# Optimization experiments

Hardware: AMD Instinct MI355X
Metric: run time of the kernel (lower is better)

## Reference

```python
import jax, jax.numpy as jnp
import numpy as np

B = 2          # number of point clouds (batch vector has B blocks)
N_PER = 16384  # points per cloud
F = 32         # input feature dim
D = 3          # coordinate dim
RATIO = 0.25
R = 0.2        # ball-query radius
K = 64         # max_neighbors
H1 = 64        # MLP hidden
COUT = 128     # MLP output
M = int(N_PER * RATIO)  # centroids per cloud


def setup_inputs() -> dict:
    key = jax.random.key(0)
    k0, k1, k2, k3 = jax.random.split(key, 4)
    x = jax.random.normal(k0, (B * N_PER, F), jnp.float32)
    pos = jax.random.uniform(k1, (B * N_PER, D), jnp.float32)
    batch = jnp.repeat(jnp.arange(B), N_PER)
    W1 = jax.random.normal(k2, (F + D, H1), jnp.float32) / np.sqrt(F + D)
    b1 = jnp.zeros((H1,), jnp.float32)
    W2 = jax.random.normal(k3, (H1, COUT), jnp.float32) / np.sqrt(H1)
    b2 = jnp.zeros((COUT,), jnp.float32)
    return {"x": x, "pos": pos, "batch": batch, "W1": W1, "b1": b1, "W2": W2, "b2": b2}


def _fps(pos_b):
    """Iterative farthest point sampling: (N_PER, D) -> (M,) indices."""
    d0 = jnp.sum((pos_b - pos_b[0]) ** 2, axis=-1)  # start at point 0

    def body(d, _):
        i = jnp.argmax(d)
        d = jnp.minimum(d, jnp.sum((pos_b - pos_b[i]) ** 2, axis=-1))
        return d, i

    _, idxs = jax.lax.scan(body, d0, None, length=M - 1)
    return jnp.concatenate([jnp.zeros((1,), idxs.dtype), idxs])


def _set_abstraction(x_b, pos_b, W1, b1, W2, b2):
    idx = _fps(pos_b)            # (M,)
    pc = pos_b[idx]              # centroid positions (M, D)
    # ball query: squared distances centroids -> all points, capped at K neighbors
    d2 = jnp.sum((pc[:, None, :] - pos_b[None, :, :]) ** 2, axis=-1)  # (M, N_PER)
    neg = jnp.where(d2 <= R * R, -d2, -jnp.inf)
    vals, nbr = jax.lax.top_k(neg, K)        # K nearest within radius
    valid = vals > -jnp.inf                  # (M, K)
    xj = x_b[nbr]                            # (M, K, F)
    pj = pos_b[nbr]                          # (M, K, D)
    # faithful to source: msg = pos_j - pos_i / r  (note: pos_i/r, not (pos_j-pos_i)/r)
    msg = jnp.concatenate([xj, pj - pc[:, None, :] / R], axis=-1)  # (M, K, F+D)
    h = jax.nn.relu(msg @ W1 + b1) @ W2 + b2                       # (M, K, COUT)
    h = jnp.where(valid[:, :, None], h, -jnp.inf)
    out = jnp.max(h, axis=1)                 # max aggregation over neighbors
    out = jnp.where(jnp.isfinite(out), out, 0.0)
    return out, pc


def reference(x, pos, batch, W1, b1, W2, b2):
    xb = x.reshape(B, N_PER, F)
    pb = pos.reshape(B, N_PER, D)
    out, pc = jax.vmap(lambda xx, pp: _set_abstraction(xx, pp, W1, b1, W2, b2))(xb, pb)
    batch_out = jnp.repeat(jnp.arange(B, dtype=batch.dtype), M)
    return out.reshape(B * M, COUT), pc.reshape(B * M, D), batch_out
```

## Files before the change

kernel.cpp:

```cpp
#include <hip/hip_runtime.h>
#include <hip/hip_bf16.h>

#define NPTS 16384
#define MCENT 4096
#define BCLD 2
#define FDIM 32
#define H1DIM 64
#define CODIM 128
#define KNBR 64
#define R2CUT 0.04f

__device__ __forceinline__ float d2e(float ax, float ay, float az,
                                     float bx, float by, float bz) {
  float dx = __fsub_rn(ax, bx);
  float dy = __fsub_rn(ay, by);
  float dz = __fsub_rn(az, bz);
  return __fadd_rn(__fadd_rn(__fmul_rn(dx, dx), __fmul_rn(dy, dy)), __fmul_rn(dz, dz));
}

__device__ __forceinline__ int spread3(int v) {
  return ((v & 4) << 4) | ((v & 2) << 2) | (v & 1);
}
__device__ __forceinline__ int cell_of(float x, float y, float z) {
  int cx = min(7, (int)(x * 8.0f));
  int cy = min(7, (int)(y * 8.0f));
  int cz = min(7, (int)(z * 8.0f));
  return (spread3(cx) << 2) | (spread3(cy) << 1) | spread3(cz);
}

#define DPP_LEXMAX_STEP(bb, nn, ctrl)                                          \
  do {                                                                         \
    unsigned _ob = (unsigned)__builtin_amdgcn_update_dpp(0, (int)(bb), ctrl,   \
                                                         0xf, 0xf, false);     \
    unsigned _on = (unsigned)__builtin_amdgcn_update_dpp(0, (int)(nn), ctrl,   \
                                                         0xf, 0xf, false);     \
    bool _t = (_ob > (bb)) || (_ob == (bb) && _on > (nn));                     \
    (bb) = _t ? _ob : (bb);                                                    \
    (nn) = _t ? _on : (nn);                                                    \
  } while (0)

__device__ __forceinline__ int rdlane(int v, int l) {
  return __builtin_amdgcn_readlane(v, l);
}
__device__ __forceinline__ float rdlanef(float v, int l) {
  return __int_as_float(__builtin_amdgcn_readlane(__float_as_int(v), l));
}

__global__ __launch_bounds__(1024) void fps_kernel(const float* __restrict__ pos,
                                                   int* __restrict__ fps_idx,
                                                   float4* __restrict__ ws_sorted) {
  const int b = blockIdx.x;
  const float* P = pos + (size_t)b * NPTS * 3;
  float4* S = ws_sorted + (size_t)b * NPTS;
  const int tid = threadIdx.x;
  const int lane = tid & 63;
  const int wave = tid >> 6;

  __shared__ int hist[512];
  __shared__ int offs[512];
  __shared__ unsigned long long skey[2][16];
  __shared__ float4 spos[2][16];
  __shared__ int winners[MCENT];

  if (tid < 512) hist[tid] = 0;
  __syncthreads();
#pragma unroll 4
  for (int j = 0; j < 16; ++j) {
    int i = tid + j * 1024;
    float x = P[3 * i + 0], y = P[3 * i + 1], z = P[3 * i + 2];
    atomicAdd(&hist[cell_of(x, y, z)], 1);
  }
  __syncthreads();
  if (tid < 64) {
    int base = tid * 8;
    int loc[8];
    int run = 0;
#pragma unroll
    for (int k = 0; k < 8; ++k) { loc[k] = run; run += hist[base + k]; }
    int inc = run;
#pragma unroll
    for (int off = 1; off < 64; off <<= 1) {
      int o = __shfl_up(inc, off);
      if (tid >= off) inc += o;
    }
    int ex = inc - run;
#pragma unroll
    for (int k = 0; k < 8; ++k) offs[base + k] = ex + loc[k];
  }
  __syncthreads();
#pragma unroll 4
  for (int j = 0; j < 16; ++j) {
    int i = tid + j * 1024;
    float x = P[3 * i + 0], y = P[3 * i + 1], z = P[3 * i + 2];
    int p = atomicAdd(&offs[cell_of(x, y, z)], 1);
    S[p] = make_float4(x, y, z, __int_as_float(i));
  }
  __syncthreads();

  float px[16], py[16], pz[16], d[16];
  unsigned nidx[16];
  const float x0 = P[0], y0 = P[1], z0 = P[2];
  float bxm, bxM, bym, byM, bzm, bzM;
  unsigned tb = 0u, tn = 0u;
  float tx = 0.f, ty = 0.f, tz = 0.f;
#pragma unroll
  for (int j = 0; j < 16; ++j) {
    float4 v = S[tid * 16 + j];
    px[j] = v.x; py[j] = v.y; pz[j] = v.z;
    nidx[j] = ~(unsigned)__float_as_int(v.w);
    float dj = d2e(v.x, v.y, v.z, x0, y0, z0);
    d[j] = dj;
    if (j == 0) {
      bxm = v.x; bxM = v.x; bym = v.y; byM = v.y; bzm = v.z; bzM = v.z;
    } else {
      bxm = fminf(bxm, v.x); bxM = fmaxf(bxM, v.x);
      bym = fminf(bym, v.y); byM = fmaxf(byM, v.y);
      bzm = fminf(bzm, v.z); bzM = fmaxf(bzM, v.z);
    }
    unsigned db = __float_as_uint(dj);
    unsigned nj = nidx[j];
    bool t = (db > tb) || (db == tb && nj > tn);
    tb = t ? db : tb; tn = t ? nj : tn;
    tx = t ? v.x : tx; ty = t ? v.y : ty; tz = t ? v.z : tz;
  }

  if (tid == 0) winners[0] = 0;

  bool wavedirty = true;
  unsigned cwb = 0u, cwn = 0u;
  float cwx = 0.f, cwy = 0.f, cwz = 0.f;

  for (int m = 1; m < MCENT; ++m) {
    const int par = m & 1;

    if (wavedirty) {
      unsigned bb = tb, nn = tn;
      DPP_LEXMAX_STEP(bb, nn, 0x111);
      DPP_LEXMAX_STEP(bb, nn, 0x112);
      DPP_LEXMAX_STEP(bb, nn, 0x114);
      DPP_LEXMAX_STEP(bb, nn, 0x118);
      DPP_LEXMAX_STEP(bb, nn, 0x142);
      DPP_LEXMAX_STEP(bb, nn, 0x143);
      cwb = (unsigned)rdlane((int)bb, 63);
      cwn = (unsigned)rdlane((int)nn, 63);
      unsigned long long own = __ballot(tb == cwb && tn == cwn);
      int ol = (int)__ffsll(own) - 1;
      cwx = rdlanef(tx, ol);
      cwy = rdlanef(ty, ol);
      cwz = rdlanef(tz, ol);
    }
    if (lane == 0) {
      skey[par][wave] = ((unsigned long long)cwb << 32) | (unsigned long long)cwn;
      spos[par][wave] = make_float4(cwx, cwy, cwz, 0.0f);
    }
    __syncthreads();

    unsigned rb, rn;
    unsigned sb0 = 0u, sn0 = 0u;
    {
      unsigned bb = 0u, nn = 0u;
      if (lane < 16) {
        unsigned long long kk = skey[par][lane];
        bb = (unsigned)(kk >> 32);
        nn = (unsigned)kk;
        sb0 = bb; sn0 = nn;
        DPP_LEXMAX_STEP(bb, nn, 0x111);
        DPP_LEXMAX_STEP(bb, nn, 0x112);
        DPP_LEXMAX_STEP(bb, nn, 0x114);
        DPP_LEXMAX_STEP(bb, nn, 0x118);
      }
      rb = (unsigned)rdlane((int)bb, 15);
      rn = (unsigned)rdlane((int)nn, 15);
    }
    unsigned long long wm = __ballot(lane < 16 && sb0 == rb && sn0 == rn);
    int ws = (int)__ffsll(wm) - 1;
    float4 wp = spos[par][ws];
    if (tid == 0) winners[m] = (int)(~rn);

    float ex = fmaxf(fmaxf(bxm - wp.x, wp.x - bxM), 0.0f);
    float ey = fmaxf(fmaxf(bym - wp.y, wp.y - byM), 0.0f);
    float ez = fmaxf(fmaxf(bzm - wp.z, wp.z - bzM), 0.0f);
    float lb = (ex * ex + ey * ey + ez * ez) * 0.999f;
    bool mydirty = lb < __uint_as_float(tb);
    if (mydirty) {
      unsigned nb = 0u, nn2 = 0u;
      float nx = 0.f, ny = 0.f, nz = 0.f;
#pragma unroll
      for (int j = 0; j < 16; ++j) {
        float dj = fminf(d[j], d2e(px[j], py[j], pz[j], wp.x, wp.y, wp.z));
        d[j] = dj;
        unsigned db = __float_as_uint(dj);
        unsigned nj = nidx[j];
        bool t = (db > nb) || (db == nb && nj > nn2);
        nb = t ? db : nb; nn2 = t ? nj : nn2;
        nx = t ? px[j] : nx; ny = t ? py[j] : ny; nz = t ? pz[j] : nz;
      }
      tb = nb; tn = nn2; tx = nx; ty = ny; tz = nz;
    }
    wavedirty = (__ballot(mydirty) != 0ULL);
  }

  __syncthreads();
  for (int i = tid; i < MCENT; i += 1024) fps_idx[b * MCENT + i] = winners[i];
}

__global__ __launch_bounds__(256) void ballq_kernel(const float* __restrict__ pos,
                                                    const int* __restrict__ fps_idx,
                                                    int* __restrict__ nbr,
                                                    float* __restrict__ out_pc,
                                                    float* __restrict__ out_batch) {
  const int wave = threadIdx.x >> 6;
  const int lane = threadIdx.x & 63;
  const int c = blockIdx.x * 4 + wave;
  const int b = c >> 12;
  const float* P = pos + (size_t)b * NPTS * 3;

  const int ci = fps_idx[c];
  const float cx = P[3 * ci + 0];
  const float cy = P[3 * ci + 1];
  const float cz = P[3 * ci + 2];
  if (lane == 0) {
    out_pc[3 * c + 0] = cx;
    out_pc[3 * c + 1] = cy;
    out_pc[3 * c + 2] = cz;
    out_batch[c] = (float)b;
  }

  __shared__ unsigned long long list[4][1024];
  __shared__ int cnt[4];
  if (lane == 0) cnt[wave] = 0;

  for (int i = lane; i < NPTS; i += 64) {
    const float qx = P[3 * i + 0];
    const float qy = P[3 * i + 1];
    const float qz = P[3 * i + 2];
    const float dd = d2e(cx, cy, cz, qx, qy, qz);
    if (dd <= R2CUT) {
      int p = atomicAdd(&cnt[wave], 1);
      if (p < 1024)
        list[wave][p] = ((unsigned long long)__float_as_uint(dd) << 32)
                      | (unsigned long long)(unsigned)i;
    }
  }
  __syncthreads();

  int n = cnt[wave];
  if (n > 1024) n = 1024;

  unsigned long long loc[16];
#pragma unroll
  for (int k = 0; k < 16; ++k) {
    int i = lane + k * 64;
    loc[k] = (i < n) ? list[wave][i] : ~0ULL;
  }
  unsigned long long mv = loc[0];
#pragma unroll
  for (int k = 1; k < 16; ++k)
    if (loc[k] < mv) mv = loc[k];

  int myout = -1;
  for (int s = 0; s < 64; ++s) {
    unsigned long long wmin = mv;
#pragma unroll
    for (int off = 32; off >= 1; off >>= 1) {
      unsigned long long o = __shfl_xor(wmin, off);
      if (o < wmin) wmin = o;
    }
    if (lane == s) myout = (wmin == ~0ULL) ? -1 : (int)(unsigned)wmin;
    if (mv == wmin && wmin != ~0ULL) {
#pragma unroll
      for (int k = 0; k < 16; ++k)
        if (loc[k] == wmin) loc[k] = ~0ULL;
      mv = loc[0];
#pragma unroll
      for (int k = 1; k < 16; ++k)
        if (loc[k] < mv) mv = loc[k];
    }
  }
  nbr[c * KNBR + lane] = myout;
}

__global__ __launch_bounds__(256) void mlp_kernel(const float* __restrict__ pos,
                                                  const float* __restrict__ x,
                                                  const int* __restrict__ fps_idx,
                                                  const int* __restrict__ nbr,
                                                  const float* __restrict__ W1,
                                                  const float* __restrict__ b1,
                                                  const float* __restrict__ W2,
                                                  const float* __restrict__ b2,
                                                  float* __restrict__ out) {
  const int c = blockIdx.x;
  const int b = c >> 12;
  const float* P = pos + (size_t)b * NPTS * 3;
  const float* X = x + (size_t)b * NPTS * FDIM;

  __shared__ float W1s[35 * 64];
  __shared__ float W2s[64 * 128];
  __shared__ float b1s[64];
  __shared__ float b2s[128];
  __shared__ float h1s[64][64];
  __shared__ float pmax[2][128];
  __shared__ int validk[64];

  const int tid = threadIdx.x;
  for (int i = tid; i < 35 * 64; i += 256) W1s[i] = W1[i];
  for (int i = tid; i < 64 * 128; i += 256) W2s[i] = W2[i];
  if (tid < 64) b1s[tid] = b1[tid];
  else if (tid < 192) b2s[tid - 64] = b2[tid - 64];

  const int ci = fps_idx[c];
  const float c5x = P[3 * ci + 0] / 0.2f;
  const float c5y = P[3 * ci + 1] / 0.2f;
  const float c5z = P[3 * ci + 2] / 0.2f;

  const int k = tid >> 2, q = tid & 3;
  const int nk = nbr[c * KNBR + k];
  if (q == 0) validk[k] = (nk >= 0) ? 1 : 0;
  const int nkc = (nk < 0) ? 0 : nk;

  float msg[35];
  const float4* Xr = (const float4*)(X + (size_t)nkc * FDIM);
#pragma unroll
  for (int i4 = 0; i4 < 8; ++i4) {
    float4 v = Xr[i4];
    msg[i4 * 4 + 0] = v.x; msg[i4 * 4 + 1] = v.y;
    msg[i4 * 4 + 2] = v.z; msg[i4 * 4 + 3] = v.w;
  }
  msg[32] = P[3 * nkc + 0] - c5x;
  msg[33] = P[3 * nkc + 1] - c5y;
  msg[34] = P[3 * nkc + 2] - c5z;

  __syncthreads();

  float acc[16];
#pragma unroll
  for (int h = 0; h < 16; ++h) acc[h] = b1s[q * 16 + h];
#pragma unroll
  for (int i = 0; i < 35; ++i) {
    const float m = msg[i];
    const float4* wrow = (const float4*)&W1s[i * 64 + q * 16];
#pragma unroll
    for (int j4 = 0; j4 < 4; ++j4) {
      float4 w = wrow[j4];
      acc[j4 * 4 + 0] += m * w.x;
      acc[j4 * 4 + 1] += m * w.y;
      acc[j4 * 4 + 2] += m * w.z;
      acc[j4 * 4 + 3] += m * w.w;
    }
  }
#pragma unroll
  for (int h = 0; h < 16; ++h) h1s[k][q * 16 + h] = fmaxf(acc[h], 0.0f);
  __syncthreads();

  const int ch = tid & 127, half = tid >> 7;
  float w2r[64];
#pragma unroll
  for (int i = 0; i < 64; ++i) w2r[i] = W2s[i * 128 + ch];

  float mx = -INFINITY;
  for (int k2 = half * 32; k2 < half * 32 + 32; ++k2) {
    if (!validk[k2]) continue;
    float s = b2s[ch];
    const float4* hr = (const float4*)h1s[k2];
#pragma unroll
    for (int i4 = 0; i4 < 16; ++i4) {
      float4 h4 = hr[i4];
      s += h4.x * w2r[i4 * 4 + 0] + h4.y * w2r[i4 * 4 + 1]
         + h4.z * w2r[i4 * 4 + 2] + h4.w * w2r[i4 * 4 + 3];
    }
    mx = fmaxf(mx, s);
  }
  pmax[half][ch] = mx;
  __syncthreads();

  if (tid < 128) {
    float m2 = fmaxf(pmax[0][tid], pmax[1][tid]);
    out[(size_t)c * CODIM + tid] = (m2 > -INFINITY) ? m2 : 0.0f;
  }
}

extern "C" void kernel_launch(void* const* d_in, const int* in_sizes, int n_in,
                              void* d_out, int out_size, void* d_ws, size_t ws_size,
                              hipStream_t stream) {
  const float* x   = (const float*)d_in[0];
  const float* pos = (const float*)d_in[1];
  const float* W1  = (const float*)d_in[3];
  const float* b1  = (const float*)d_in[4];
  const float* W2  = (const float*)d_in[5];
  const float* b2  = (const float*)d_in[6];
  float* out = (float*)d_out;

  int* fps_idx = (int*)d_ws;
  int* nbr     = (int*)d_ws + BCLD * MCENT;
  float4* ws_sorted = (float4*)nbr;

  float* out_pc    = out + (size_t)BCLD * MCENT * CODIM;
  float* out_batch = out_pc + (size_t)BCLD * MCENT * 3;

  hipLaunchKernelGGL(fps_kernel, dim3(BCLD), dim3(1024), 0, stream, pos, fps_idx, ws_sorted);
  hipLaunchKernelGGL(ballq_kernel, dim3(BCLD * MCENT / 4), dim3(256), 0, stream,
                     pos, fps_idx, nbr, out_pc, out_batch);
  hipLaunchKernelGGL(mlp_kernel, dim3(BCLD * MCENT), dim3(256), 0, stream,
                     pos, x, fps_idx, nbr, W1, b1, W2, b2, out);
}
```

Baseline: 7.661 ms.

## Shrink FPS block to 256 threads with 64 points per thread in sub-boxes

The farthest-point-sampling kernel now runs 256 threads (4 waves) per cloud instead of 1024, each thread holding 64 sorted points split into four 16-point sub-blocks, each with its own bounding box and cached max. The cross-wave reduction per iteration shrinks from 16 to 4 entries, aiming to cut barrier and LDS reduction cost on the serial 4095-step loop, and per-sub-block bounding-box pruning skips distance updates for distant sub-blocks. Point indices are packed as 16-bit values to save registers. In exchange each thread does more sequential work when its sub-blocks are dirty, and register pressure is much higher (64-element arrays), which risks spills.

```diff
diff --git a/kernel.cpp b/kernel.cpp
--- a/kernel.cpp
+++ b/kernel.cpp
@@ -46,9 +46,9 @@
   return __int_as_float(__builtin_amdgcn_readlane(__float_as_int(v), l));
 }
 
-__global__ __launch_bounds__(1024) void fps_kernel(const float* __restrict__ pos,
-                                                   int* __restrict__ fps_idx,
-                                                   float4* __restrict__ ws_sorted) {
+__global__ __launch_bounds__(256, 1) void fps_kernel(const float* __restrict__ pos,
+                                                     int* __restrict__ fps_idx,
+                                                     float4* __restrict__ ws_sorted) {
   const int b = blockIdx.x;
   const float* P = pos + (size_t)b * NPTS * 3;
   float4* S = ws_sorted + (size_t)b * NPTS;
@@ -58,15 +58,16 @@
 
   __shared__ int hist[512];
   __shared__ int offs[512];
-  __shared__ unsigned long long skey[2][16];
-  __shared__ float4 spos[2][16];
+  __shared__ unsigned long long skey[2][4];
+  __shared__ float4 spos[2][4];
   __shared__ int winners[MCENT];
 
-  if (tid < 512) hist[tid] = 0;
+  hist[tid] = 0;
+  hist[tid + 256] = 0;
   __syncthreads();
 #pragma unroll 4
-  for (int j = 0; j < 16; ++j) {
-    int i = tid + j * 1024;
+  for (int j = 0; j < 64; ++j) {
+    int i = tid + j * 256;
     float x = P[3 * i + 0], y = P[3 * i + 1], z = P[3 * i + 2];
     atomicAdd(&hist[cell_of(x, y, z)], 1);
   }
@@ -89,39 +90,61 @@
   }
   __syncthreads();
 #pragma unroll 4
-  for (int j = 0; j < 16; ++j) {
-    int i = tid + j * 1024;
+  for (int j = 0; j < 64; ++j) {
+    int i = tid + j * 256;
     float x = P[3 * i + 0], y = P[3 * i + 1], z = P[3 * i + 2];
     int p = atomicAdd(&offs[cell_of(x, y, z)], 1);
     S[p] = make_float4(x, y, z, __int_as_float(i));
   }
   __syncthreads();
 
-  float px[16], py[16], pz[16], d[16];
-  unsigned nidx[16];
+  float px[64], py[64], pz[64], d[64];
+  unsigned npk[32];
+  unsigned long long skmax[4];
+  float sbxm[4], sbxM[4], sbym[4], sbyM[4], sbzm[4], sbzM[4];
+  float spxr[4], spyr[4], spzr[4];
   const float x0 = P[0], y0 = P[1], z0 = P[2];
-  float bxm, bxM, bym, byM, bzm, bzM;
-  unsigned tb = 0u, tn = 0u;
-  float tx = 0.f, ty = 0.f, tz = 0.f;
-#pragma unroll
-  for (int j = 0; j < 16; ++j) {
-    float4 v = S[tid * 16 + j];
-    px[j] = v.x; py[j] = v.y; pz[j] = v.z;
-    nidx[j] = ~(unsigned)__float_as_int(v.w);
-    float dj = d2e(v.x, v.y, v.z, x0, y0, z0);
-    d[j] = dj;
-    if (j == 0) {
-      bxm = v.x; bxM = v.x; bym = v.y; byM = v.y; bzm = v.z; bzM = v.z;
-    } else {
-      bxm = fminf(bxm, v.x); bxM = fmaxf(bxM, v.x);
-      bym = fminf(bym, v.y); byM = fmaxf(byM, v.y);
-      bzm = fminf(bzm, v.z); bzM = fmaxf(bzM, v.z);
-    }
-    unsigned db = __float_as_uint(dj);
-    unsigned nj = nidx[j];
-    bool t = (db > tb) || (db == tb && nj > tn);
-    tb = t ? db : tb; tn = t ? nj : tn;
-    tx = t ? v.x : tx; ty = t ? v.y : ty; tz = t ? v.z : tz;
+
+#pragma unroll
+  for (int s = 0; s < 4; ++s) {
+    unsigned sb = 0u, sn = 0u;
+    float sx = 0.f, sy = 0.f, sz = 0.f;
+    float xm = 1e30f, xM = -1e30f, ym = 1e30f, yM = -1e30f, zm = 1e30f, zM = -1e30f;
+#pragma unroll
+    for (int t = 0; t < 16; ++t) {
+      const int j = s * 16 + t;
+      float4 v = S[tid * 64 + j];
+      px[j] = v.x; py[j] = v.y; pz[j] = v.z;
+      unsigned nj = ~(unsigned)__float_as_int(v.w);
+      if ((j & 1) == 0) npk[j >> 1] = nj & 0xFFFFu;
+      else npk[j >> 1] |= (nj & 0xFFFFu) << 16;
+      float dj = d2e(v.x, v.y, v.z, x0, y0, z0);
+      d[j] = dj;
+      xm = fminf(xm, v.x); xM = fmaxf(xM, v.x);
+      ym = fminf(ym, v.y); yM = fmaxf(yM, v.y);
+      zm = fminf(zm, v.z); zM = fmaxf(zM, v.z);
+      unsigned db = __float_as_uint(dj);
+      bool g = (db > sb) || (db == sb && nj > sn);
+      sb = g ? db : sb; sn = g ? nj : sn;
+      sx = g ? v.x : sx; sy = g ? v.y : sy; sz = g ? v.z : sz;
+    }
+    skmax[s] = ((unsigned long long)sb << 32) | sn;
+    sbxm[s] = xm; sbxM[s] = xM; sbym[s] = ym; sbyM[s] = yM; sbzm[s] = zm; sbzM[s] = zM;
+    spxr[s] = sx; spyr[s] = sy; spzr[s] = sz;
+  }
+
+  unsigned tkb, tkn;
+  float tx, ty, tz;
+  {
+    unsigned long long k = skmax[0];
+    float ax = spxr[0], ay = spyr[0], az = spzr[0];
+#pragma unroll
+    for (int s = 1; s < 4; ++s) {
+      bool g = skmax[s] > k;
+      k = g ? skmax[s] : k;
+      ax = g ? spxr[s] : ax; ay = g ? spyr[s] : ay; az = g ? spzr[s] : az;
+    }
+    tkb = (unsigned)(k >> 32); tkn = (unsigned)k; tx = ax; ty = ay; tz = az;
   }
 
   if (tid == 0) winners[0] = 0;
@@ -134,7 +157,7 @@
     const int par = m & 1;
 
     if (wavedirty) {
-      unsigned bb = tb, nn = tn;
+      unsigned bb = tkb, nn = tkn;
       DPP_LEXMAX_STEP(bb, nn, 0x111);
       DPP_LEXMAX_STEP(bb, nn, 0x112);
       DPP_LEXMAX_STEP(bb, nn, 0x114);
@@ -143,7 +166,7 @@
       DPP_LEXMAX_STEP(bb, nn, 0x143);
       cwb = (unsigned)rdlane((int)bb, 63);
       cwn = (unsigned)rdlane((int)nn, 63);
-      unsigned long long own = __ballot(tb == cwb && tn == cwn);
+      unsigned long long own = __ballot(tkb == cwb && tkn == cwn);
       int ol = (int)__ffsll(own) - 1;
       cwx = rdlanef(tx, ol);
       cwy = rdlanef(ty, ol);
@@ -159,49 +182,64 @@
     unsigned sb0 = 0u, sn0 = 0u;
     {
       unsigned bb = 0u, nn = 0u;
-      if (lane < 16) {
+      if (lane < 4) {
         unsigned long long kk = skey[par][lane];
         bb = (unsigned)(kk >> 32);
         nn = (unsigned)kk;
         sb0 = bb; sn0 = nn;
         DPP_LEXMAX_STEP(bb, nn, 0x111);
         DPP_LEXMAX_STEP(bb, nn, 0x112);
-        DPP_LEXMAX_STEP(bb, nn, 0x114);
-        DPP_LEXMAX_STEP(bb, nn, 0x118);
       }
-      rb = (unsigned)rdlane((int)bb, 15);
-      rn = (unsigned)rdlane((int)nn, 15);
-    }
-    unsigned long long wm = __ballot(lane < 16 && sb0 == rb && sn0 == rn);
+      rb = (unsigned)rdlane((int)bb, 3);
+      rn = (unsigned)rdlane((int)nn, 3);
+    }
+    unsigned long long wm = __ballot(lane < 4 && sb0 == rb && sn0 == rn);
     int ws = (int)__ffsll(wm) - 1;
     float4 wp = spos[par][ws];
     if (tid == 0) winners[m] = (int)(~rn);
 
-    float ex = fmaxf(fmaxf(bxm - wp.x, wp.x - bxM), 0.0f);
-    float ey = fmaxf(fmaxf(bym - wp.y, wp.y - byM), 0.0f);
-    float ez = fmaxf(fmaxf(bzm - wp.z, wp.z - bzM), 0.0f);
-    float lb = (ex * ex + ey * ey + ez * ez) * 0.999f;
-    bool mydirty = lb < __uint_as_float(tb);
+    bool mydirty = false;
+#pragma unroll
+    for (int s = 0; s < 4; ++s) {
+      float ex = fmaxf(fmaxf(sbxm[s] - wp.x, wp.x - sbxM[s]), 0.0f);
+      float ey = fmaxf(fmaxf(sbym[s] - wp.y, wp.y - sbyM[s]), 0.0f);
+      float ez = fmaxf(fmaxf(sbzm[s] - wp.z, wp.z - sbzM[s]), 0.0f);
+      float lb = (ex * ex + ey * ey + ez * ez) * 0.999f;
+      if (lb < __uint_as_float((unsigned)(skmax[s] >> 32))) {
+        mydirty = true;
+        unsigned nb = 0u, nn2 = 0u;
+        float nx = 0.f, ny = 0.f, nz = 0.f;
+#pragma unroll
+        for (int t = 0; t < 16; ++t) {
+          const int j = s * 16 + t;
+          float dj = fminf(d[j], d2e(px[j], py[j], pz[j], wp.x, wp.y, wp.z));
+          d[j] = dj;
+          unsigned db = __float_as_uint(dj);
+          unsigned nj = 0xFFFF0000u | ((npk[j >> 1] >> ((j & 1) * 16)) & 0xFFFFu);
+          bool g = (db > nb) || (db == nb && nj > nn2);
+          nb = g ? db : nb; nn2 = g ? nj : nn2;
+          nx = g ? px[j] : nx; ny = g ? py[j] : ny; nz = g ? pz[j] : nz;
+        }
+        skmax[s] = ((unsigned long long)nb << 32) | nn2;
+        spxr[s] = nx; spyr[s] = ny; spzr[s] = nz;
+      }
+    }
     if (mydirty) {
-      unsigned nb = 0u, nn2 = 0u;
-      float nx = 0.f, ny = 0.f, nz = 0.f;
-#pragma unroll
-      for (int j = 0; j < 16; ++j) {
-        float dj = fminf(d[j], d2e(px[j], py[j], pz[j], wp.x, wp.y, wp.z));
-        d[j] = dj;
-        unsigned db = __float_as_uint(dj);
-        unsigned nj = nidx[j];
-        bool t = (db > nb) || (db == nb && nj > nn2);
-        nb = t ? db : nb; nn2 = t ? nj : nn2;
-        nx = t ? px[j] : nx; ny = t ? py[j] : ny; nz = t ? pz[j] : nz;
+      unsigned long long k = skmax[0];
+      float ax = spxr[0], ay = spyr[0], az = spzr[0];
+#pragma unroll
+      for (int s = 1; s < 4; ++s) {
+        bool g = skmax[s] > k;
+        k = g ? skmax[s] : k;
+        ax = g ? spxr[s] : ax; ay = g ? spyr[s] : ay; az = g ? spzr[s] : az;
       }
-      tb = nb; tn = nn2; tx = nx; ty = ny; tz = nz;
+      tkb = (unsigned)(k >> 32); tkn = (unsigned)k; tx = ax; ty = ay; tz = az;
     }
     wavedirty = (__ballot(mydirty) != 0ULL);
   }
 
   __syncthreads();
-  for (int i = tid; i < MCENT; i += 1024) fps_idx[b * MCENT + i] = winners[i];
+  for (int i = tid; i < MCENT; i += 256) fps_idx[b * MCENT + i] = winners[i];
 }
 
 __global__ __launch_bounds__(256) void ballq_kernel(const float* __restrict__ pos,
@@ -397,7 +435,7 @@
   float* out_pc    = out + (size_t)BCLD * MCENT * CODIM;
   float* out_batch = out_pc + (size_t)BCLD * MCENT * 3;
 
-  hipLaunchKernelGGL(fps_kernel, dim3(BCLD), dim3(1024), 0, stream, pos, fps_idx, ws_sorted);
+  hipLaunchKernelGGL(fps_kernel, dim3(BCLD), dim3(256), 0, stream, pos, fps_idx, ws_sorted);
   hipLaunchKernelGGL(ballq_kernel, dim3(BCLD * MCENT / 4), dim3(256), 0, stream,
                      pos, fps_idx, nbr, out_pc, out_batch);
   hipLaunchKernelGGL(mlp_kernel, dim3(BCLD * MCENT), dim3(256), 0, stream,
```

Result: slower. 29.81 ms (+289.1%).

## Split FPS into sort kernel and single-wave FPS with lazy subset updates

Applied to the files above, without the earlier changes.

Farthest point sampling moves from a 1024-thread block that needs a __syncthreads per iteration to a single 64-lane wave per cloud. Distances live in LDS, and each lane tracks two 128-point spatially sorted subsets with bounding boxes. Each iteration recomputes only the subsets whose box lower bound says the new centroid can shrink their maximum, so block-wide barriers and most distance updates are skipped. The trade-off is that one wave per cloud leaves almost the whole GPU idle, and dirty subsets are processed one at a time in a serial loop. That could be slower if many subsets need updating per iteration.

```diff
diff --git a/kernel.cpp b/kernel.cpp
--- a/kernel.cpp
+++ b/kernel.cpp
@@ -39,6 +39,16 @@
     (nn) = _t ? _on : (nn);                                                    \
   } while (0)
 
+#define DPP_LEXMAX_FULL(bb, nn)                                                \
+  do {                                                                         \
+    DPP_LEXMAX_STEP(bb, nn, 0x111);                            \
+    DPP_LEXMAX_STEP(bb, nn, 0x112);                            \
+    DPP_LEXMAX_STEP(bb, nn, 0x114);                            \
+    DPP_LEXMAX_STEP(bb, nn, 0x118);                            \
+    DPP_LEXMAX_STEP(bb, nn, 0x142);                          \
+    DPP_LEXMAX_STEP(bb, nn, 0x143);   \
+  } while (0)
+
 __device__ __forceinline__ int rdlane(int v, int l) {
   return __builtin_amdgcn_readlane(v, l);
 }
@@ -46,21 +56,17 @@
   return __int_as_float(__builtin_amdgcn_readlane(__float_as_int(v), l));
 }
 
-__global__ __launch_bounds__(1024) void fps_kernel(const float* __restrict__ pos,
-                                                   int* __restrict__ fps_idx,
-                                                   float4* __restrict__ ws_sorted) {
+__global__ __launch_bounds__(1024) void sort_kernel(const float* __restrict__ pos,
+                                                    float4* __restrict__ Sall,
+                                                    unsigned* __restrict__ umeta,
+                                                    float* __restrict__ fmeta) {
   const int b = blockIdx.x;
   const float* P = pos + (size_t)b * NPTS * 3;
-  float4* S = ws_sorted + (size_t)b * NPTS;
+  float4* S = Sall + (size_t)b * NPTS;
   const int tid = threadIdx.x;
-  const int lane = tid & 63;
-  const int wave = tid >> 6;
 
   __shared__ int hist[512];
   __shared__ int offs[512];
-  __shared__ unsigned long long skey[2][16];
-  __shared__ float4 spos[2][16];
-  __shared__ int winners[MCENT];
 
   if (tid < 512) hist[tid] = 0;
   __syncthreads();
@@ -97,111 +103,147 @@
   }
   __syncthreads();
 
-  float px[16], py[16], pz[16], d[16];
-  unsigned nidx[16];
+  if (tid < 128) {
+    const float x0 = P[0], y0 = P[1], z0 = P[2];
+    unsigned kb = 0u, kn = 0u;
+    float bpx = 0.f, bpy = 0.f, bpz = 0.f;
+    float xm = 1e30f, xM = -1e30f, ym = 1e30f, yM = -1e30f, zm = 1e30f, zM = -1e30f;
+    const float4* Ss = S + tid * 128;
+    for (int t = 0; t < 128; ++t) {
+      float4 v = Ss[t];
+      float dj = d2e(v.x, v.y, v.z, x0, y0, z0);
+      xm = fminf(xm, v.x); xM = fmaxf(xM, v.x);
+      ym = fminf(ym, v.y); yM = fmaxf(yM, v.y);
+      zm = fminf(zm, v.z); zM = fmaxf(zM, v.z);
+      unsigned db = __float_as_uint(dj);
+      unsigned nj = ~(unsigned)__float_as_int(v.w);
+      bool g = (db > kb) || (db == kb && nj > kn);
+      kb = g ? db : kb; kn = g ? nj : kn;
+      bpx = g ? v.x : bpx; bpy = g ? v.y : bpy; bpz = g ? v.z : bpz;
+    }
+    const int gi = b * 128 + tid;
+    umeta[0 * 256 + gi] = kb;
+    umeta[1 * 256 + gi] = kn;
+    fmeta[0 * 256 + gi] = bpx;
+    fmeta[1 * 256 + gi] = bpy;
+    fmeta[2 * 256 + gi] = bpz;
+    fmeta[3 * 256 + gi] = xm;
+    fmeta[4 * 256 + gi] = xM;
+    fmeta[5 * 256 + gi] = ym;
+    fmeta[6 * 256 + gi] = yM;
+    fmeta[7 * 256 + gi] = zm;
+    fmeta[8 * 256 + gi] = zM;
+  }
+}
+
+__global__ __launch_bounds__(64) void fps_wave(const float* __restrict__ pos,
+                                               int* __restrict__ fps_idx,
+                                               const float4* __restrict__ Sall,
+                                               const unsigned* __restrict__ umeta,
+                                               const float* __restrict__ fmeta) {
+  const int b = blockIdx.x;
+  const int lane = threadIdx.x;
+  const float* P = pos + (size_t)b * NPTS * 3;
+  const float4* Sb = Sall + (size_t)b * NPTS;
+
+  __shared__ float dL[NPTS];
+
   const float x0 = P[0], y0 = P[1], z0 = P[2];
-  float bxm, bxM, bym, byM, bzm, bzM;
-  unsigned tb = 0u, tn = 0u;
-  float tx = 0.f, ty = 0.f, tz = 0.f;
-#pragma unroll
-  for (int j = 0; j < 16; ++j) {
-    float4 v = S[tid * 16 + j];
-    px[j] = v.x; py[j] = v.y; pz[j] = v.z;
-    nidx[j] = ~(unsigned)__float_as_int(v.w);
-    float dj = d2e(v.x, v.y, v.z, x0, y0, z0);
-    d[j] = dj;
-    if (j == 0) {
-      bxm = v.x; bxM = v.x; bym = v.y; byM = v.y; bzm = v.z; bzM = v.z;
-    } else {
-      bxm = fminf(bxm, v.x); bxM = fmaxf(bxM, v.x);
-      bym = fminf(bym, v.y); byM = fmaxf(byM, v.y);
-      bzm = fminf(bzm, v.z); bzM = fmaxf(bzM, v.z);
-    }
-    unsigned db = __float_as_uint(dj);
-    unsigned nj = nidx[j];
-    bool t = (db > tb) || (db == tb && nj > tn);
-    tb = t ? db : tb; tn = t ? nj : tn;
-    tx = t ? v.x : tx; ty = t ? v.y : ty; tz = t ? v.z : tz;
-  }
-
-  if (tid == 0) winners[0] = 0;
-
-  bool wavedirty = true;
-  unsigned cwb = 0u, cwn = 0u;
-  float cwx = 0.f, cwy = 0.f, cwz = 0.f;
+#pragma unroll 4
+  for (int it = 0; it < 256; ++it) {
+    int i = it * 64 + lane;
+    float4 v = Sb[i];
+    dL[i] = d2e(v.x, v.y, v.z, x0, y0, z0);
+  }
+
+  unsigned skb[2], skn[2];
+  float spx[2], spy[2], spz[2];
+  float bxm[2], bxM[2], bym[2], byM[2], bzm[2], bzM[2];
+#pragma unroll
+  for (int s2 = 0; s2 < 2; ++s2) {
+    const int gi = b * 128 + lane * 2 + s2;
+    skb[s2] = umeta[0 * 256 + gi];
+    skn[s2] = umeta[1 * 256 + gi];
+    spx[s2] = fmeta[0 * 256 + gi];
+    spy[s2] = fmeta[1 * 256 + gi];
+    spz[s2] = fmeta[2 * 256 + gi];
+    bxm[s2] = fmeta[3 * 256 + gi];
+    bxM[s2] = fmeta[4 * 256 + gi];
+    bym[s2] = fmeta[5 * 256 + gi];
+    byM[s2] = fmeta[6 * 256 + gi];
+    bzm[s2] = fmeta[7 * 256 + gi];
+    bzM[s2] = fmeta[8 * 256 + gi];
+  }
+
+  if (lane == 0) fps_idx[b * MCENT] = 0;
 
   for (int m = 1; m < MCENT; ++m) {
-    const int par = m & 1;
-
-    if (wavedirty) {
-      unsigned bb = tb, nn = tn;
-      DPP_LEXMAX_STEP(bb, nn, 0x111);
-      DPP_LEXMAX_STEP(bb, nn, 0x112);
-      DPP_LEXMAX_STEP(bb, nn, 0x114);
-      DPP_LEXMAX_STEP(bb, nn, 0x118);
-      DPP_LEXMAX_STEP(bb, nn, 0x142);
-      DPP_LEXMAX_STEP(bb, nn, 0x143);
-      cwb = (unsigned)rdlane((int)bb, 63);
-      cwn = (unsigned)rdlane((int)nn, 63);
-      unsigned long long own = __ballot(tb == cwb && tn == cwn);
-      int ol = (int)__ffsll(own) - 1;
-      cwx = rdlanef(tx, ol);
-      cwy = rdlanef(ty, ol);
-      cwz = rdlanef(tz, ol);
-    }
-    if (lane == 0) {
-      skey[par][wave] = ((unsigned long long)cwb << 32) | (unsigned long long)cwn;
-      spos[par][wave] = make_float4(cwx, cwy, cwz, 0.0f);
-    }
-    __syncthreads();
-
-    unsigned rb, rn;
-    unsigned sb0 = 0u, sn0 = 0u;
-    {
-      unsigned bb = 0u, nn = 0u;
-      if (lane < 16) {
-        unsigned long long kk = skey[par][lane];
-        bb = (unsigned)(kk >> 32);
-        nn = (unsigned)kk;
-        sb0 = bb; sn0 = nn;
-        DPP_LEXMAX_STEP(bb, nn, 0x111);
-        DPP_LEXMAX_STEP(bb, nn, 0x112);
-        DPP_LEXMAX_STEP(bb, nn, 0x114);
-        DPP_LEXMAX_STEP(bb, nn, 0x118);
+    bool g2 = (skb[1] > skb[0]) || (skb[1] == skb[0] && skn[1] > skn[0]);
+    unsigned lkb = g2 ? skb[1] : skb[0];
+    unsigned lkn = g2 ? skn[1] : skn[0];
+    float lpx = g2 ? spx[1] : spx[0];
+    float lpy = g2 ? spy[1] : spy[0];
+    float lpz = g2 ? spz[1] : spz[0];
+
+    unsigned bb = lkb, nn = lkn;
+    DPP_LEXMAX_FULL(bb, nn);
+    const unsigned Whi = (unsigned)rdlane((int)bb, 63);
+    const unsigned Wlo = (unsigned)rdlane((int)nn, 63);
+    if (lane == 0) fps_idx[b * MCENT + m] = (int)(~Wlo);
+
+    unsigned long long own = __ballot(lkb == Whi && lkn == Wlo);
+    const int ol = (int)__ffsll(own) - 1;
+    const float wx = rdlanef(lpx, ol);
+    const float wy = rdlanef(lpy, ol);
+    const float wz = rdlanef(lpz, ol);
+
+    unsigned dm = 0u;
+#pragma unroll
+    for (int s2 = 0; s2 < 2; ++s2) {
+      float ex = fmaxf(fmaxf(bxm[s2] - wx, wx - bxM[s2]), 0.0f);
+      float ey = fmaxf(fmaxf(bym[s2] - wy, wy - byM[s2]), 0.0f);
+      float ez = fmaxf(fmaxf(bzm[s2] - wz, wz - bzM[s2]), 0.0f);
+      float lb = (ex * ex + ey * ey + ez * ez) * 0.999f;
+      if (lb < __uint_as_float(skb[s2])) dm |= (1u << s2);
+    }
+
+    unsigned long long anyb = __ballot(dm != 0u);
+    while (anyb) {
+      const int L = (int)__ffsll(anyb) - 1;
+      const unsigned f = (unsigned)rdlane((int)dm, L);
+      const int sl = (f & 1u) ? 0 : 1;
+      const int Ssub = L * 2 + sl;
+      const int pt = Ssub * 128 + lane;
+      float4 v0 = Sb[pt];
+      float4 v1 = Sb[pt + 64];
+      float n0 = fminf(dL[pt],      d2e(v0.x, v0.y, v0.z, wx, wy, wz));
+      float n1 = fminf(dL[pt + 64], d2e(v1.x, v1.y, v1.z, wx, wy, wz));
+      dL[pt] = n0;
+      dL[pt + 64] = n1;
+      unsigned c0b = __float_as_uint(n0), c0n = ~(unsigned)__float_as_int(v0.w);
+      unsigned c1b = __float_as_uint(n1), c1n = ~(unsigned)__float_as_int(v1.w);
+      bool gg = (c1b > c0b) || (c1b == c0b && c1n > c0n);
+      unsigned cb = gg ? c1b : c0b, cn = gg ? c1n : c0n;
+      float cx = gg ? v1.x : v0.x;
+      float cy = gg ? v1.y : v0.y;
+      float cz = gg ? v1.z : v0.z;
+      unsigned b2 = cb, n2 = cn;
+      DPP_LEXMAX_FULL(b2, n2);
+      const unsigned nhi = (unsigned)rdlane((int)b2, 63);
+      const unsigned nlo = (unsigned)rdlane((int)n2, 63);
+      unsigned long long mmk = __ballot(cb == nhi && cn == nlo);
+      const int fl = (int)__ffsll(mmk) - 1;
+      const float nx = rdlanef(cx, fl);
+      const float ny = rdlanef(cy, fl);
+      const float nz = rdlanef(cz, fl);
+      if (lane == L) {
+        skb[sl] = nhi; skn[sl] = nlo;
+        spx[sl] = nx; spy[sl] = ny; spz[sl] = nz;
+        dm &= ~(1u << sl);
       }
-      rb = (unsigned)rdlane((int)bb, 15);
-      rn = (unsigned)rdlane((int)nn, 15);
-    }
-    unsigned long long wm = __ballot(lane < 16 && sb0 == rb && sn0 == rn);
-    int ws = (int)__ffsll(wm) - 1;
-    float4 wp = spos[par][ws];
-    if (tid == 0) winners[m] = (int)(~rn);
-
-    float ex = fmaxf(fmaxf(bxm - wp.x, wp.x - bxM), 0.0f);
-    float ey = fmaxf(fmaxf(bym - wp.y, wp.y - byM), 0.0f);
-    float ez = fmaxf(fmaxf(bzm - wp.z, wp.z - bzM), 0.0f);
-    float lb = (ex * ex + ey * ey + ez * ez) * 0.999f;
-    bool mydirty = lb < __uint_as_float(tb);
-    if (mydirty) {
-      unsigned nb = 0u, nn2 = 0u;
-      float nx = 0.f, ny = 0.f, nz = 0.f;
-#pragma unroll
-      for (int j = 0; j < 16; ++j) {
-        float dj = fminf(d[j], d2e(px[j], py[j], pz[j], wp.x, wp.y, wp.z));
-        d[j] = dj;
-        unsigned db = __float_as_uint(dj);
-        unsigned nj = nidx[j];
-        bool t = (db > nb) || (db == nb && nj > nn2);
-        nb = t ? db : nb; nn2 = t ? nj : nn2;
-        nx = t ? px[j] : nx; ny = t ? py[j] : ny; nz = t ? pz[j] : nz;
-      }
-      tb = nb; tn = nn2; tx = nx; ty = ny; tz = nz;
-    }
-    wavedirty = (__ballot(mydirty) != 0ULL);
-  }
-
-  __syncthreads();
-  for (int i = tid; i < MCENT; i += 1024) fps_idx[b * MCENT + i] = winners[i];
+      anyb = __ballot(dm != 0u);
+    }
+  }
 }
 
 __global__ __launch_bounds__(256) void ballq_kernel(const float* __restrict__ pos,
@@ -391,13 +433,19 @@
   float* out = (float*)d_out;
 
   int* fps_idx = (int*)d_ws;
-  int* nbr     = (int*)d_ws + BCLD * MCENT;
-  float4* ws_sorted = (float4*)nbr;
+  char* region = (char*)d_ws + (size_t)BCLD * MCENT * 4;
+  int* nbr = (int*)region;
+  float4* S = (float4*)region;
+  unsigned* umeta = (unsigned*)(region + 524288);
+  float* fmeta = (float*)(region + 524288 + 2048);
 
   float* out_pc    = out + (size_t)BCLD * MCENT * CODIM;
   float* out_batch = out_pc + (size_t)BCLD * MCENT * 3;
 
-  hipLaunchKernelGGL(fps_kernel, dim3(BCLD), dim3(1024), 0, stream, pos, fps_idx, ws_sorted);
+  hipLaunchKernelGGL(sort_kernel, dim3(BCLD), dim3(1024), 0, stream,
+                     pos, S, umeta, fmeta);
+  hipLaunchKernelGGL(fps_wave, dim3(BCLD), dim3(64), 0, stream,
+                     pos, fps_idx, S, umeta, fmeta);
   hipLaunchKernelGGL(ballq_kernel, dim3(BCLD * MCENT / 4), dim3(256), 0, stream,
                      pos, fps_idx, nbr, out_pc, out_batch);
   hipLaunchKernelGGL(mlp_kernel, dim3(BCLD * MCENT), dim3(256), 0, stream,
```

Measured after the change: 18.82 ms. 2.46x slower.
